# Performance work log

Measured on AMD Instinct MI355X. Metric: run time of the kernel, lower is better.

## Reference

```python
import jax, jax.numpy as jnp
import numpy as np

B, L, DIN, H, E, K = 64, 256, 768, 64, 8, 2
S = 16  # sqrt(L): token<->feature grid side
LOSS_COEF = 1e-2


def gelu(x):
    return jax.nn.gelu(x, approximate=False)  # torch nn.GELU (exact erf)


def cv_squared(v):
    v = v.astype(jnp.float32)
    return jnp.var(v, ddof=1) / (jnp.mean(v) ** 2 + 1e-10)


def setup_inputs() -> dict:
    key = jax.random.key(0)
    ks = jax.random.split(key, 16)
    rn = lambda k, shape, s=0.02: jax.random.normal(k, shape, jnp.float32) * s
    lap = jnp.array([[0., 1., 0.], [1., -4., 1.], [0., 1., 0.]], jnp.float32)
    return {
        "x": jax.random.normal(ks[0], (B, L, DIN), jnp.float32),
        "dte": jax.random.normal(ks[1], (B, L, DIN), jnp.float32),
        "w_gate": rn(ks[2], (L, E), 1.0),
        "W_exp": rn(ks[3], (E, DIN, H)), "b_exp": jnp.zeros((E, H), jnp.float32),
        "W_sh": rn(ks[4], (DIN, H)), "b_sh": jnp.zeros((H,), jnp.float32),
        "ln_g": jnp.ones((H,), jnp.float32), "ln_b": jnp.zeros((H,), jnp.float32),
        "W_px": rn(ks[5], (H, 2 * H)), "b_px": jnp.zeros((2 * H,), jnp.float32),
        "conv_sh": jnp.tile(lap[None, None], (H, 1, 1, 1)),  # depthwise Laplacian [H,1,3,3]
        "W_pxx": rn(ks[6], (H, H)), "b_pxx": jnp.zeros((H,), jnp.float32),
        "W_dte": rn(ks[7], (H, H)), "b_dte": jnp.zeros((H,), jnp.float32),
        "W_dteall": rn(ks[8], (H, H)), "b_dteall": jnp.zeros((H,), jnp.float32),
        "W_rgb": rn(ks[9], (DIN, H)), "b_rgb": jnp.zeros((H,), jnp.float32),
        "W_fx": rn(ks[10], (H, H)), "b_fx": jnp.zeros((H,), jnp.float32),
        "W_fmod": rn(ks[11], (H, H)), "b_fmod": jnp.zeros((H,), jnp.float32),
        "W_fxx": rn(ks[12], (H, H)), "b_fxx": jnp.zeros((H,), jnp.float32),
    }


def reference(x, dte, w_gate, W_exp, b_exp, W_sh, b_sh, ln_g, ln_b, W_px, b_px,
              conv_sh, W_pxx, b_pxx, W_dte, b_dte, W_dteall, b_dteall,
              W_rgb, b_rgb, W_fx, b_fx, W_fmod, b_fmod, W_fxx, b_fxx):
    # ---- top-k gating (clean logits; noisy_gating=False / eval) ----
    logits = dte.mean(-1) @ w_gate                     # [B,E]
    topv, topi = jax.lax.top_k(logits, K)
    topg = jax.nn.softmax(topv, axis=1)
    gates = jnp.zeros_like(logits).at[jnp.arange(B)[:, None], topi].set(topg)
    importance = gates.sum(0)
    load = (gates > 0).sum(0).astype(jnp.float32)
    loss = LOSS_COEF * (cv_squared(importance) + cv_squared(load))
    # ---- sparse dispatch / expert Linear / weighted combine (dense-equivalent) ----
    y = jnp.einsum('be,bld,edh->blh', gates, dte, W_exp) + (gates @ b_exp)[:, None, :]
    # ---- shared expert Linear + Shared block ----
    sh = dte @ W_sh + b_sh                             # [B,L,H]
    shortcut = sh
    t = (sh - sh.mean(-1, keepdims=True)) * jax.lax.rsqrt(sh.var(-1, keepdims=True) + 1e-6)
    t = t * ln_g + ln_b
    t = t @ W_px + b_px                                # [B,L,2H]
    t1, t2 = t[..., :H], t[..., H:]
    f = t1.transpose(0, 2, 1).reshape(B, H, S, S)      # token2feature
    f = jax.lax.conv_general_dilated(f, conv_sh, (1, 1), 'SAME', feature_group_count=H)
    t1 = f.reshape(B, H, L).transpose(0, 2, 1)         # feature2token
    sh = (gelu(t1) * t2) @ W_pxx + b_pxx + shortcut
    # ---- combine MoE and shared streams ----
    dte_tok = (y @ W_dte + b_dte) + (sh @ W_dteall + b_dteall)
    rgb_tok = x @ W_rgb + b_rgb
    # ---- Fusion (its self.norm was overwritten to GELU; token<->feature round-trip is identity) ----
    shortcut = rgb_tok
    a = gelu(rgb_tok) @ W_fx + b_fx
    m = gelu(dte_tok) @ W_fmod + b_fmod
    out = (gelu(m) * a) @ W_fxx + b_fxx + shortcut     # [B,L,H]
    return out, loss
```

## Files before the change

kernel.cpp:

```cpp
#include <hip/hip_runtime.h>
#include <math.h>

typedef unsigned short u16;
typedef unsigned int u32;


__device__ __forceinline__ float bf2f(u16 u) {
    union { u32 i; float f; } x; x.i = ((u32)u) << 16; return x.f;
}
__device__ __forceinline__ u16 f2bf(float f) {
    union { float f; u32 i; } x; x.f = f;
    u32 i = x.i;
    return (u16)((i + 0x7fffu + ((i >> 16) & 1u)) >> 16);
}
__device__ __forceinline__ u32 pack2(float a, float b) {
    return (u32)f2bf(a) | ((u32)f2bf(b) << 16);
}
__device__ __forceinline__ float wsum(float v) {
    #pragma unroll
    for (int o = 1; o < 64; o <<= 1) v += __shfl_xor(v, o, 64);
    return v;
}
__device__ __forceinline__ float gelu_f(float x) {
    return 0.5f * x * (1.0f + erff(x * 0.70710678118654752440f));
}

__global__ __launch_bounds__(256) void k_gate_part(const float* __restrict__ dte,
                                                   const float* __restrict__ w_gate,
                                                   float* __restrict__ partial) {
    __shared__ float dmeanS[64];
    int p = blockIdx.x, tid = threadIdx.x, w = tid >> 6, lane = tid & 63;
    for (int i = 0; i < 16; i++) {
        int l = w * 16 + i;
        const float* pr = dte + ((size_t)p * 64 + l) * 768;
        float s = 0.f;
        #pragma unroll
        for (int j = 0; j < 12; j++) s += pr[j * 64 + lane];
        s = wsum(s);
        if (lane == 0) dmeanS[l] = s * (1.f / 768.f);
    }
    __syncthreads();
    if (w == 0) {
        float dm = dmeanS[lane];
        int wl = (p & 3) * 64 + lane;
        #pragma unroll
        for (int e = 0; e < 8; e++) {
            float s = wsum(dm * w_gate[wl * 8 + e]);
            if (lane == 0) partial[p * 8 + e] = s;
        }
    }
}

__global__ __launch_bounds__(256) void k_gate_fin(const float* __restrict__ partial,
                                                  const float* __restrict__ b_exp,
                                                  int* __restrict__ topi,
                                                  float* __restrict__ topg,
                                                  float* __restrict__ bias_y,
                                                  float* __restrict__ loss_out) {
    __shared__ float gS[64 * 8];
    __shared__ int i0S[64], i1S[64];
    __shared__ float g0S[64], g1S[64];
    int tid = threadIdx.x;
    if (tid < 64) {
        float lg[8];
        #pragma unroll
        for (int e = 0; e < 8; e++)
            lg[e] = partial[(tid * 4 + 0) * 8 + e] + partial[(tid * 4 + 1) * 8 + e] +
                    partial[(tid * 4 + 2) * 8 + e] + partial[(tid * 4 + 3) * 8 + e];
        int i0 = 0; float v0 = lg[0];
        #pragma unroll
        for (int e = 1; e < 8; e++) if (lg[e] > v0) { v0 = lg[e]; i0 = e; }
        int i1 = -1; float v1 = -1e30f;
        #pragma unroll
        for (int e = 0; e < 8; e++) if (e != i0 && lg[e] > v1) { v1 = lg[e]; i1 = e; }
        if (i1 < 0) i1 = (i0 + 1) & 7;
        float e2 = expf(v1 - v0);
        float g0 = 1.f / (1.f + e2);
        float g1 = e2 / (1.f + e2);
        #pragma unroll
        for (int e = 0; e < 8; e++) gS[tid * 8 + e] = 0.f;
        gS[tid * 8 + i0] = g0;
        gS[tid * 8 + i1] = g1;
        i0S[tid] = i0; i1S[tid] = i1; g0S[tid] = g0; g1S[tid] = g1;
        topi[tid * 2] = i0; topi[tid * 2 + 1] = i1;
        topg[tid * 2] = g0; topg[tid * 2 + 1] = g1;
    }
    __syncthreads();
    for (int idx = tid; idx < 4096; idx += 256) {
        int b = idx >> 6, h = idx & 63;
        bias_y[idx] = g0S[b] * b_exp[i0S[b] * 64 + h] + g1S[b] * b_exp[i1S[b] * 64 + h];
    }
    if (tid < 64) {
        float g[8];
        #pragma unroll
        for (int e = 0; e < 8; e++) g[e] = gS[tid * 8 + e];
        float imp[8], ld[8];
        #pragma unroll
        for (int e = 0; e < 8; e++) {
            imp[e] = wsum(g[e]);
            ld[e]  = wsum(g[e] > 0.f ? 1.f : 0.f);
        }
        if (tid == 0) {
            float l = 0.f;
            {
                float s = 0.f;
                #pragma unroll
                for (int e = 0; e < 8; e++) s += imp[e];
                float mn = s / 8.f, v = 0.f;
                #pragma unroll
                for (int e = 0; e < 8; e++) { float d = imp[e] - mn; v += d * d; }
                l += (v / 7.f) / (mn * mn + 1e-10f);
            }
            {
                float s = 0.f;
                #pragma unroll
                for (int e = 0; e < 8; e++) s += ld[e];
                float mn = s / 8.f, v = 0.f;
                #pragma unroll
                for (int e = 0; e < 8; e++) { float d = ld[e] - mn; v += d * d; }
                l += (v / 7.f) / (mn * mn + 1e-10f);
            }
            loss_out[0] = 0.01f * l;
        }
    }
}

__global__ __launch_bounds__(256) void k_gemm3(const float* __restrict__ dte,
                                               const float* __restrict__ x,
                                               const float* __restrict__ W_sh,
                                               const float* __restrict__ b_sh,
                                               const float* __restrict__ W_exp,
                                               const int* __restrict__ topi,
                                               const float* __restrict__ topg,
                                               const float* __restrict__ bias_y,
                                               const float* __restrict__ W_rgb,
                                               const float* __restrict__ b_rgb,
                                               float* __restrict__ buf_sh,
                                               u16* __restrict__ buf_y,
                                               float* __restrict__ out_rgb) {
    __shared__ float As[64 * 68];
    __shared__ float Ws[64 * 68];
    int bid = blockIdx.x;
    int kind = bid >> 8;
    int row0 = (bid & 255) * 64;
    int b = row0 >> 8;
    int tid = threadIdx.x, rg = tid >> 4, cg = tid & 15;
    const float* A = (kind == 2) ? x : dte;
    const float* W0 = (kind == 2) ? W_rgb : W_sh;
    const float* W1 = W0;
    float g0 = 0.f, g1 = 0.f;
    if (kind == 1) {
        W0 = W_exp + (size_t)topi[2 * b] * 49152;
        W1 = W_exp + (size_t)topi[2 * b + 1] * 49152;
        g0 = topg[2 * b]; g1 = topg[2 * b + 1];
    }
    float acc[4][4] = {};
    for (int kc = 0; kc < 12; kc++) {
        __syncthreads();
        #pragma unroll
        for (int j = 0; j < 4; j++) {
            int e4 = tid + j * 256;
            int r = e4 >> 4, kq = e4 & 15;
            *(float4*)(As + r * 68 + kq * 4) =
                *(const float4*)(A + (size_t)(row0 + r) * 768 + kc * 64 + kq * 4);
        }
        #pragma unroll
        for (int j = 0; j < 4; j++) {
            int e4 = tid + j * 256;
            int k = e4 >> 4, hq = e4 & 15;
            size_t off = (size_t)(kc * 64 + k) * 64 + hq * 4;
            float4 wv;
            if (kind == 1) {
                float4 a = *(const float4*)(W0 + off);
                float4 c = *(const float4*)(W1 + off);
                wv.x = g0 * a.x + g1 * c.x; wv.y = g0 * a.y + g1 * c.y;
                wv.z = g0 * a.z + g1 * c.z; wv.w = g0 * a.w + g1 * c.w;
            } else {
                wv = *(const float4*)(W0 + off);
            }
            *(float4*)(Ws + k * 68 + hq * 4) = wv;
        }
        __syncthreads();
        const float* ar = As + rg * 4 * 68;
        #pragma unroll 8
        for (int kk = 0; kk < 64; kk++) {
            float a0 = ar[kk], a1 = ar[68 + kk], a2 = ar[136 + kk], a3 = ar[204 + kk];
            float4 wv = *(const float4*)(Ws + kk * 68 + cg * 4);
            acc[0][0] += a0 * wv.x; acc[0][1] += a0 * wv.y; acc[0][2] += a0 * wv.z; acc[0][3] += a0 * wv.w;
            acc[1][0] += a1 * wv.x; acc[1][1] += a1 * wv.y; acc[1][2] += a1 * wv.z; acc[1][3] += a1 * wv.w;
            acc[2][0] += a2 * wv.x; acc[2][1] += a2 * wv.y; acc[2][2] += a2 * wv.z; acc[2][3] += a2 * wv.w;
            acc[3][0] += a3 * wv.x; acc[3][1] += a3 * wv.y; acc[3][2] += a3 * wv.z; acc[3][3] += a3 * wv.w;
        }
    }
    if (kind == 0) {
        float4 bs = *(const float4*)(b_sh + cg * 4);
        #pragma unroll
        for (int i = 0; i < 4; i++) {
            int r = row0 + rg * 4 + i;
            *(float4*)(buf_sh + (size_t)r * 64 + cg * 4) =
                make_float4(acc[i][0] + bs.x, acc[i][1] + bs.y, acc[i][2] + bs.z, acc[i][3] + bs.w);
        }
    } else if (kind == 1) {
        float4 by = *(const float4*)(bias_y + b * 64 + cg * 4);
        #pragma unroll
        for (int i = 0; i < 4; i++) {
            int r = row0 + rg * 4 + i;
            u32* dst = (u32*)(buf_y + (size_t)r * 64 + cg * 4);
            dst[0] = pack2(acc[i][0] + by.x, acc[i][1] + by.y);
            dst[1] = pack2(acc[i][2] + by.z, acc[i][3] + by.w);
        }
    } else {
        float4 br = *(const float4*)(b_rgb + cg * 4);
        #pragma unroll
        for (int i = 0; i < 4; i++) {
            int r = row0 + rg * 4 + i;
            *(float4*)(out_rgb + (size_t)r * 64 + cg * 4) =
                make_float4(acc[i][0] + br.x, acc[i][1] + br.y, acc[i][2] + br.z, acc[i][3] + br.w);
        }
    }
}

__global__ __launch_bounds__(256) void k_lnpx(const float* __restrict__ buf_sh,
                                              const float* __restrict__ ln_g,
                                              const float* __restrict__ ln_b,
                                              const float* __restrict__ W_px,
                                              const float* __restrict__ b_px,
                                              u16* __restrict__ t1, u16* __restrict__ t2) {
    __shared__ float T[32 * 68];
    __shared__ float Wpx[8192];
    int r0 = blockIdx.x * 32;
    int tid = threadIdx.x, w = tid >> 6, lane = tid & 63;
    #pragma unroll
    for (int j = 0; j < 8; j++) {
        int e4 = tid + j * 256;
        *(float4*)(Wpx + e4 * 4) = *(const float4*)(W_px + e4 * 4);
    }
    float lnG = ln_g[lane], lnB = ln_b[lane];
    for (int i = 0; i < 8; i++) {
        int l = w * 8 + i;
        float v = buf_sh[(size_t)(r0 + l) * 64 + lane];
        float mean = wsum(v) * (1.f / 64.f);
        float d = v - mean;
        float var = wsum(d * d) * (1.f / 64.f);
        T[l * 68 + lane] = d * rsqrtf(var + 1e-6f) * lnG + lnB;
    }
    __syncthreads();
    int rg = tid >> 4, cg = tid & 15;
    float acc1[2][4] = {}, acc2[2][4] = {};
    const float* tr = T + rg * 2 * 68;
    #pragma unroll 4
    for (int kk = 0; kk < 64; kk++) {
        float a0 = tr[kk], a1 = tr[68 + kk];
        float4 w1 = *(const float4*)(Wpx + kk * 128 + cg * 4);
        float4 w2 = *(const float4*)(Wpx + kk * 128 + 64 + cg * 4);
        acc1[0][0] += a0 * w1.x; acc1[0][1] += a0 * w1.y; acc1[0][2] += a0 * w1.z; acc1[0][3] += a0 * w1.w;
        acc1[1][0] += a1 * w1.x; acc1[1][1] += a1 * w1.y; acc1[1][2] += a1 * w1.z; acc1[1][3] += a1 * w1.w;
        acc2[0][0] += a0 * w2.x; acc2[0][1] += a0 * w2.y; acc2[0][2] += a0 * w2.z; acc2[0][3] += a0 * w2.w;
        acc2[1][0] += a1 * w2.x; acc2[1][1] += a1 * w2.y; acc2[1][2] += a1 * w2.z; acc2[1][3] += a1 * w2.w;
    }
    float4 b1 = *(const float4*)(b_px + cg * 4);
    float4 b2 = *(const float4*)(b_px + 64 + cg * 4);
    #pragma unroll
    for (int i = 0; i < 2; i++) {
        int r = r0 + rg * 2 + i;
        u32* d1 = (u32*)(t1 + (size_t)r * 64 + cg * 4);
        d1[0] = pack2(acc1[i][0] + b1.x, acc1[i][1] + b1.y);
        d1[1] = pack2(acc1[i][2] + b1.z, acc1[i][3] + b1.w);
        u32* d2 = (u32*)(t2 + (size_t)r * 64 + cg * 4);
        d2[0] = pack2(acc2[i][0] + b2.x, acc2[i][1] + b2.y);
        d2[1] = pack2(acc2[i][2] + b2.z, acc2[i][3] + b2.w);
    }
}

__global__ __launch_bounds__(256) void k_tail(const u16* __restrict__ t1,
                                              const u16* __restrict__ t2,
                                              const float* __restrict__ conv_sh,
                                              const float* __restrict__ W_pxx,
                                              const float* __restrict__ b_pxx,
                                              const float* __restrict__ buf_sh,
                                              const u16* __restrict__ buf_y,
                                              const float* __restrict__ W_dte,
                                              const float* __restrict__ b_dte,
                                              const float* __restrict__ W_dteall,
                                              const float* __restrict__ b_dteall,
                                              const float* __restrict__ W_fx,
                                              const float* __restrict__ b_fx,
                                              const float* __restrict__ W_fmod,
                                              const float* __restrict__ b_fmod,
                                              const float* __restrict__ W_fxx,
                                              const float* __restrict__ b_fxx,
                                              float* __restrict__ out) {
    __shared__ float B0[32 * 68];
    __shared__ float B1[32 * 68];
    __shared__ float B2[32 * 68];
    __shared__ float RS[32 * 64];
    int r0 = blockIdx.x * 32;
    int tid = threadIdx.x, w = tid >> 6, lane = tid & 63;
    int rg = tid >> 4, cg = tid & 15;

    {
        float c0 = conv_sh[lane * 9 + 0], c1 = conv_sh[lane * 9 + 1], c2 = conv_sh[lane * 9 + 2];
        float c3 = conv_sh[lane * 9 + 3], c4 = conv_sh[lane * 9 + 4], c5 = conv_sh[lane * 9 + 5];
        float c6 = conv_sh[lane * 9 + 6], c7 = conv_sh[lane * 9 + 7], c8 = conv_sh[lane * 9 + 8];
        for (int i = 0; i < 8; i++) {
            int l = w * 8 + i;
            int gr = r0 + l;
            int pix = gr & 255, ii = pix >> 4, jj = pix & 15;
            const u16* p = t1 + (size_t)gr * 64 + lane;
            float c = c4 * bf2f(p[0]);
            if (ii > 0) {
                c += c1 * bf2f(p[-1024]);
                if (jj > 0)  c += c0 * bf2f(p[-1024 - 64]);
                if (jj < 15) c += c2 * bf2f(p[-1024 + 64]);
            }
            if (jj > 0)  c += c3 * bf2f(p[-64]);
            if (jj < 15) c += c5 * bf2f(p[64]);
            if (ii < 15) {
                c += c7 * bf2f(p[1024]);
                if (jj > 0)  c += c6 * bf2f(p[1024 - 64]);
                if (jj < 15) c += c8 * bf2f(p[1024 + 64]);
            }
            B0[l * 68 + lane] = gelu_f(c) * bf2f(t2[(size_t)gr * 64 + lane]);
        }
    }
    __syncthreads();

    {
        float acc[2][4] = {};
        const float* ur = B0 + rg * 2 * 68;
        #pragma unroll 8
        for (int kk = 0; kk < 64; kk++) {
            float a0 = ur[kk], a1 = ur[68 + kk];
            float4 wv = *(const float4*)(W_pxx + kk * 64 + cg * 4);
            acc[0][0] += a0 * wv.x; acc[0][1] += a0 * wv.y; acc[0][2] += a0 * wv.z; acc[0][3] += a0 * wv.w;
            acc[1][0] += a1 * wv.x; acc[1][1] += a1 * wv.y; acc[1][2] += a1 * wv.z; acc[1][3] += a1 * wv.w;
        }
        float4 bp = *(const float4*)(b_pxx + cg * 4);
        #pragma unroll
        for (int i = 0; i < 2; i++) {
            int lr = rg * 2 + i;
            float4 shv = *(const float4*)(buf_sh + (size_t)(r0 + lr) * 64 + cg * 4);
            *(float4*)(B1 + lr * 68 + cg * 4) =
                make_float4(acc[i][0] + bp.x + shv.x, acc[i][1] + bp.y + shv.y,
                            acc[i][2] + bp.z + shv.z, acc[i][3] + bp.w + shv.w);
        }
    }
    __syncthreads();

    #pragma unroll
    for (int j = 0; j < 8; j++) {
        int e = tid + j * 256;
        int l = e >> 6, c = e & 63;
        B0[l * 68 + c] = bf2f(buf_y[(size_t)(r0 + l) * 64 + c]);
    }
    __syncthreads();

    {
        float acc[2][4] = {};
        const float* yr = B0 + rg * 2 * 68;
        const float* sr = B1 + rg * 2 * 68;
        #pragma unroll 4
        for (int kk = 0; kk < 64; kk++) {
            float y0 = yr[kk], y1 = yr[68 + kk];
            float s0 = sr[kk], s1 = sr[68 + kk];
            float4 w1 = *(const float4*)(W_dte + kk * 64 + cg * 4);
            float4 w2 = *(const float4*)(W_dteall + kk * 64 + cg * 4);
            acc[0][0] += y0 * w1.x + s0 * w2.x; acc[0][1] += y0 * w1.y + s0 * w2.y;
            acc[0][2] += y0 * w1.z + s0 * w2.z; acc[0][3] += y0 * w1.w + s0 * w2.w;
            acc[1][0] += y1 * w1.x + s1 * w2.x; acc[1][1] += y1 * w1.y + s1 * w2.y;
            acc[1][2] += y1 * w1.z + s1 * w2.z; acc[1][3] += y1 * w1.w + s1 * w2.w;
        }
        float4 bd1 = *(const float4*)(b_dte + cg * 4);
        float4 bd2 = *(const float4*)(b_dteall + cg * 4);
        #pragma unroll
        for (int i = 0; i < 2; i++) {
            int lr = rg * 2 + i;
            *(float4*)(B2 + lr * 68 + cg * 4) =
                make_float4(gelu_f(acc[i][0] + bd1.x + bd2.x), gelu_f(acc[i][1] + bd1.y + bd2.y),
                            gelu_f(acc[i][2] + bd1.z + bd2.z), gelu_f(acc[i][3] + bd1.w + bd2.w));
        }
    }
    __syncthreads();

    #pragma unroll
    for (int j = 0; j < 2; j++) {
        int e4 = tid + j * 256;
        int l = e4 >> 4, c4i = e4 & 15;
        float4 rv = *(const float4*)(out + (size_t)(r0 + l) * 64 + c4i * 4);
        *(float4*)(RS + l * 64 + c4i * 4) = rv;
        B1[l * 68 + c4i * 4 + 0] = gelu_f(rv.x);
        B1[l * 68 + c4i * 4 + 1] = gelu_f(rv.y);
        B1[l * 68 + c4i * 4 + 2] = gelu_f(rv.z);
        B1[l * 68 + c4i * 4 + 3] = gelu_f(rv.w);
    }
    __syncthreads();

    {
        float accA[2][4] = {}, accM[2][4] = {};
        const float* ga = B1 + rg * 2 * 68;
        const float* gm = B2 + rg * 2 * 68;
        #pragma unroll 4
        for (int kk = 0; kk < 64; kk++) {
            float a0 = ga[kk], a1 = ga[68 + kk];
            float m0 = gm[kk], m1 = gm[68 + kk];
            float4 wa = *(const float4*)(W_fx + kk * 64 + cg * 4);
            float4 wm = *(const float4*)(W_fmod + kk * 64 + cg * 4);
            accA[0][0] += a0 * wa.x; accA[0][1] += a0 * wa.y; accA[0][2] += a0 * wa.z; accA[0][3] += a0 * wa.w;
            accA[1][0] += a1 * wa.x; accA[1][1] += a1 * wa.y; accA[1][2] += a1 * wa.z; accA[1][3] += a1 * wa.w;
            accM[0][0] += m0 * wm.x; accM[0][1] += m0 * wm.y; accM[0][2] += m0 * wm.z; accM[0][3] += m0 * wm.w;
            accM[1][0] += m1 * wm.x; accM[1][1] += m1 * wm.y; accM[1][2] += m1 * wm.z; accM[1][3] += m1 * wm.w;
        }
        float4 bx = *(const float4*)(b_fx + cg * 4);
        float4 bm = *(const float4*)(b_fmod + cg * 4);
        #pragma unroll
        for (int i = 0; i < 2; i++) {
            int lr = rg * 2 + i;
            float a0 = accA[i][0] + bx.x, a1 = accA[i][1] + bx.y, a2 = accA[i][2] + bx.z, a3 = accA[i][3] + bx.w;
            float m0 = accM[i][0] + bm.x, m1 = accM[i][1] + bm.y, m2 = accM[i][2] + bm.z, m3 = accM[i][3] + bm.w;
            *(float4*)(B0 + lr * 68 + cg * 4) =
                make_float4(gelu_f(m0) * a0, gelu_f(m1) * a1, gelu_f(m2) * a2, gelu_f(m3) * a3);
        }
    }
    __syncthreads();

    {
        float acc[2][4] = {};
        const float* pr = B0 + rg * 2 * 68;
        #pragma unroll 8
        for (int kk = 0; kk < 64; kk++) {
            float p0 = pr[kk], p1 = pr[68 + kk];
            float4 wv = *(const float4*)(W_fxx + kk * 64 + cg * 4);
            acc[0][0] += p0 * wv.x; acc[0][1] += p0 * wv.y; acc[0][2] += p0 * wv.z; acc[0][3] += p0 * wv.w;
            acc[1][0] += p1 * wv.x; acc[1][1] += p1 * wv.y; acc[1][2] += p1 * wv.z; acc[1][3] += p1 * wv.w;
        }
        float4 bo = *(const float4*)(b_fxx + cg * 4);
        #pragma unroll
        for (int i = 0; i < 2; i++) {
            int lr = rg * 2 + i;
            *(float4*)(out + (size_t)(r0 + lr) * 64 + cg * 4) =
                make_float4(acc[i][0] + bo.x + RS[lr * 64 + cg * 4 + 0],
                            acc[i][1] + bo.y + RS[lr * 64 + cg * 4 + 1],
                            acc[i][2] + bo.z + RS[lr * 64 + cg * 4 + 2],
                            acc[i][3] + bo.w + RS[lr * 64 + cg * 4 + 3]);
        }
    }
}

extern "C" void kernel_launch(void* const* d_in, const int* in_sizes, int n_in,
                              void* d_out, int out_size, void* d_ws, size_t ws_size,
                              hipStream_t stream) {
    const float* x       = (const float*)d_in[0];
    const float* dte     = (const float*)d_in[1];
    const float* w_gate  = (const float*)d_in[2];
    const float* W_exp   = (const float*)d_in[3];
    const float* b_exp   = (const float*)d_in[4];
    const float* W_sh    = (const float*)d_in[5];
    const float* b_sh    = (const float*)d_in[6];
    const float* ln_g    = (const float*)d_in[7];
    const float* ln_b    = (const float*)d_in[8];
    const float* W_px    = (const float*)d_in[9];
    const float* b_px    = (const float*)d_in[10];
    const float* conv_sh = (const float*)d_in[11];
    const float* W_pxx   = (const float*)d_in[12];
    const float* b_pxx   = (const float*)d_in[13];
    const float* W_dte   = (const float*)d_in[14];
    const float* b_dte   = (const float*)d_in[15];
    const float* W_dteall= (const float*)d_in[16];
    const float* b_dteall= (const float*)d_in[17];
    const float* W_rgb   = (const float*)d_in[18];
    const float* b_rgb   = (const float*)d_in[19];
    const float* W_fx    = (const float*)d_in[20];
    const float* b_fx    = (const float*)d_in[21];
    const float* W_fmod  = (const float*)d_in[22];
    const float* b_fmod  = (const float*)d_in[23];
    const float* W_fxx   = (const float*)d_in[24];
    const float* b_fxx   = (const float*)d_in[25];

    float* out = (float*)d_out;

    float* wsf    = (float*)d_ws;
    float* partial= wsf;
    int*   topi   = (int*)(wsf + 2048);
    float* topg   = wsf + 2176;
    float* bias_y = wsf + 2304;
    float* buf_sh = wsf + 8192;
    u16*   buf_y  = (u16*)(wsf + 8192 + 1048576);
    u16*   t1     = (u16*)(wsf + 8192 + 1048576 + 524288);
    u16*   t2     = (u16*)(wsf + 8192 + 1048576 + 524288*2);

    hipLaunchKernelGGL(k_gate_part, dim3(256), dim3(256), 0, stream, dte, w_gate, partial);
    hipLaunchKernelGGL(k_gate_fin, dim3(1), dim3(256), 0, stream,
                       partial, b_exp, topi, topg, bias_y, out + 1048576);
    hipLaunchKernelGGL(k_gemm3, dim3(768), dim3(256), 0, stream,
                       dte, x, W_sh, b_sh, W_exp, topi, topg, bias_y, W_rgb, b_rgb,
                       buf_sh, buf_y, out);
    hipLaunchKernelGGL(k_lnpx, dim3(512), dim3(256), 0, stream,
                       buf_sh, ln_g, ln_b, W_px, b_px, t1, t2);
    hipLaunchKernelGGL(k_tail, dim3(512), dim3(256), 0, stream,
                       t1, t2, conv_sh, W_pxx, b_pxx, buf_sh, buf_y,
                       W_dte, b_dte, W_dteall, b_dteall,
                       W_fx, b_fx, W_fmod, b_fmod, W_fxx, b_fxx, out);

    (void)in_sizes; (void)n_in; (void)out_size; (void)ws_size;
}
```

Baseline: 292.8 us.

## Use bf16 MFMA for the three big projection GEMMs and vectorize gate reduction

The fused dte/x projection GEMM (shared, mixed-expert, rgb) now converts A and W tiles to bf16 in shared memory and computes with 16x16x32 bf16 MFMA instructions instead of scalar FP32 FMAs, using a K-chunk of 32. Block ordering interleaves the shared and expert kinds. The gate-mean reduction now uses float4 loads. The FP32 GEMM is the dominant compute cost. The trade-off is reduced precision from the bf16 inputs, scalar strided stores into the transposed W tile, and twice as many sync rounds.

Measured after the change: 278.7 us. 4.8% less time.

```diff
diff --git a/kernel.cpp b/kernel.cpp
--- a/kernel.cpp
+++ b/kernel.cpp
@@ -3,6 +3,8 @@
 
 typedef unsigned short u16;
 typedef unsigned int u32;
+typedef __attribute__((ext_vector_type(8))) short bf16x8;
+typedef __attribute__((ext_vector_type(4))) float f32x4;
 
 
 __device__ __forceinline__ float bf2f(u16 u) {
@@ -35,7 +37,10 @@
         const float* pr = dte + ((size_t)p * 64 + l) * 768;
         float s = 0.f;
         #pragma unroll
-        for (int j = 0; j < 12; j++) s += pr[j * 64 + lane];
+        for (int j = 0; j < 3; j++) {
+            float4 v = *(const float4*)(pr + (lane + j * 64) * 4);
+            s += v.x + v.y + v.z + v.w;
+        }
         s = wsum(s);
         if (lane == 0) dmeanS[l] = s * (1.f / 768.f);
     }
@@ -138,13 +143,16 @@
                                                float* __restrict__ buf_sh,
                                                u16* __restrict__ buf_y,
                                                float* __restrict__ out_rgb) {
-    __shared__ float As[64 * 68];
-    __shared__ float Ws[64 * 68];
+    __shared__ u16 As[64 * 40];
+    __shared__ u16 Wt[64 * 40];
     int bid = blockIdx.x;
-    int kind = bid >> 8;
-    int row0 = (bid & 255) * 64;
+    int kind, row0;
+    if (bid < 512) { kind = bid & 1; row0 = (bid >> 1) * 64; }
+    else           { kind = 2;       row0 = (bid - 512) * 64; }
     int b = row0 >> 8;
-    int tid = threadIdx.x, rg = tid >> 4, cg = tid & 15;
+    int tid = threadIdx.x, wv = tid >> 6, lane = tid & 63;
+    int m = lane & 15, quad = lane >> 4;
+
     const float* A = (kind == 2) ? x : dte;
     const float* W0 = (kind == 2) ? W_rgb : W_sh;
     const float* W1 = W0;
@@ -154,68 +162,66 @@
         W1 = W_exp + (size_t)topi[2 * b + 1] * 49152;
         g0 = topg[2 * b]; g1 = topg[2 * b + 1];
     }
-    float acc[4][4] = {};
-    for (int kc = 0; kc < 12; kc++) {
+
+    f32x4 acc0 = {0.f, 0.f, 0.f, 0.f}, acc1 = acc0, acc2 = acc0, acc3 = acc0;
+
+    for (int kc = 0; kc < 24; kc++) {
         __syncthreads();
         #pragma unroll
-        for (int j = 0; j < 4; j++) {
+        for (int j = 0; j < 2; j++) {
             int e4 = tid + j * 256;
-            int r = e4 >> 4, kq = e4 & 15;
-            *(float4*)(As + r * 68 + kq * 4) =
-                *(const float4*)(A + (size_t)(row0 + r) * 768 + kc * 64 + kq * 4);
-        }
-        #pragma unroll
-        for (int j = 0; j < 4; j++) {
+            int r = e4 >> 3, kq = e4 & 7;
+            float4 v = *(const float4*)(A + (size_t)(row0 + r) * 768 + kc * 32 + kq * 4);
+            u32* d = (u32*)&As[r * 40 + kq * 4];
+            d[0] = pack2(v.x, v.y);
+            d[1] = pack2(v.z, v.w);
+        }
+        #pragma unroll
+        for (int j = 0; j < 2; j++) {
             int e4 = tid + j * 256;
-            int k = e4 >> 4, hq = e4 & 15;
-            size_t off = (size_t)(kc * 64 + k) * 64 + hq * 4;
-            float4 wv;
+            int k = e4 >> 4, n4 = (e4 & 15) * 4;
+            size_t off = (size_t)(kc * 32 + k) * 64 + n4;
+            float4 wvv;
             if (kind == 1) {
                 float4 a = *(const float4*)(W0 + off);
                 float4 c = *(const float4*)(W1 + off);
-                wv.x = g0 * a.x + g1 * c.x; wv.y = g0 * a.y + g1 * c.y;
-                wv.z = g0 * a.z + g1 * c.z; wv.w = g0 * a.w + g1 * c.w;
+                wvv.x = g0 * a.x + g1 * c.x; wvv.y = g0 * a.y + g1 * c.y;
+                wvv.z = g0 * a.z + g1 * c.z; wvv.w = g0 * a.w + g1 * c.w;
             } else {
-                wv = *(const float4*)(W0 + off);
+                wvv = *(const float4*)(W0 + off);
             }
-            *(float4*)(Ws + k * 68 + hq * 4) = wv;
+            Wt[(n4 + 0) * 40 + k] = f2bf(wvv.x);
+            Wt[(n4 + 1) * 40 + k] = f2bf(wvv.y);
+            Wt[(n4 + 2) * 40 + k] = f2bf(wvv.z);
+            Wt[(n4 + 3) * 40 + k] = f2bf(wvv.w);
         }
         __syncthreads();
-        const float* ar = As + rg * 4 * 68;
-        #pragma unroll 8
-        for (int kk = 0; kk < 64; kk++) {
-            float a0 = ar[kk], a1 = ar[68 + kk], a2 = ar[136 + kk], a3 = ar[204 + kk];
-            float4 wv = *(const float4*)(Ws + kk * 68 + cg * 4);
-            acc[0][0] += a0 * wv.x; acc[0][1] += a0 * wv.y; acc[0][2] += a0 * wv.z; acc[0][3] += a0 * wv.w;
-            acc[1][0] += a1 * wv.x; acc[1][1] += a1 * wv.y; acc[1][2] += a1 * wv.z; acc[1][3] += a1 * wv.w;
-            acc[2][0] += a2 * wv.x; acc[2][1] += a2 * wv.y; acc[2][2] += a2 * wv.z; acc[2][3] += a2 * wv.w;
-            acc[3][0] += a3 * wv.x; acc[3][1] += a3 * wv.y; acc[3][2] += a3 * wv.z; acc[3][3] += a3 * wv.w;
-        }
-    }
-    if (kind == 0) {
-        float4 bs = *(const float4*)(b_sh + cg * 4);
+        bf16x8 a = *(const bf16x8*)&As[(wv * 16 + m) * 40 + quad * 8];
+        bf16x8 b0 = *(const bf16x8*)&Wt[(0 * 16 + m) * 40 + quad * 8];
+        bf16x8 b1 = *(const bf16x8*)&Wt[(1 * 16 + m) * 40 + quad * 8];
+        bf16x8 b2 = *(const bf16x8*)&Wt[(2 * 16 + m) * 40 + quad * 8];
+        bf16x8 b3 = *(const bf16x8*)&Wt[(3 * 16 + m) * 40 + quad * 8];
+        acc0 = __builtin_amdgcn_mfma_f32_16x16x32_bf16(a, b0, acc0, 0, 0, 0);
+        acc1 = __builtin_amdgcn_mfma_f32_16x16x32_bf16(a, b1, acc1, 0, 0, 0);
+        acc2 = __builtin_amdgcn_mfma_f32_16x16x32_bf16(a, b2, acc2, 0, 0, 0);
+        acc3 = __builtin_amdgcn_mfma_f32_16x16x32_bf16(a, b3, acc3, 0, 0, 0);
+    }
+
+    f32x4 accs[4] = {acc0, acc1, acc2, acc3};
+    #pragma unroll
+    for (int t = 0; t < 4; t++) {
+        int col = t * 16 + m;
+        float bias;
+        if (kind == 0)      bias = b_sh[col];
+        else if (kind == 1) bias = bias_y[b * 64 + col];
+        else                bias = b_rgb[col];
         #pragma unroll
         for (int i = 0; i < 4; i++) {
-            int r = row0 + rg * 4 + i;
-            *(float4*)(buf_sh + (size_t)r * 64 + cg * 4) =
-                make_float4(acc[i][0] + bs.x, acc[i][1] + bs.y, acc[i][2] + bs.z, acc[i][3] + bs.w);
-        }
-    } else if (kind == 1) {
-        float4 by = *(const float4*)(bias_y + b * 64 + cg * 4);
-        #pragma unroll
-        for (int i = 0; i < 4; i++) {
-            int r = row0 + rg * 4 + i;
-            u32* dst = (u32*)(buf_y + (size_t)r * 64 + cg * 4);
-            dst[0] = pack2(acc[i][0] + by.x, acc[i][1] + by.y);
-            dst[1] = pack2(acc[i][2] + by.z, acc[i][3] + by.w);
-        }
-    } else {
-        float4 br = *(const float4*)(b_rgb + cg * 4);
-        #pragma unroll
-        for (int i = 0; i < 4; i++) {
-            int r = row0 + rg * 4 + i;
-            *(float4*)(out_rgb + (size_t)r * 64 + cg * 4) =
-                make_float4(acc[i][0] + br.x, acc[i][1] + br.y, acc[i][2] + br.z, acc[i][3] + br.w);
+            int r = row0 + wv * 16 + quad * 4 + i;
+            float val = accs[t][i] + bias;
+            if (kind == 0)      buf_sh[(size_t)r * 64 + col] = val;
+            else if (kind == 1) buf_y[(size_t)r * 64 + col] = f2bf(val);
+            else                out_rgb[(size_t)r * 64 + col] = val;
         }
     }
 }
@@ -331,9 +337,9 @@
         #pragma unroll 8
         for (int kk = 0; kk < 64; kk++) {
             float a0 = ur[kk], a1 = ur[68 + kk];
-            float4 wv = *(const float4*)(W_pxx + kk * 64 + cg * 4);
-            acc[0][0] += a0 * wv.x; acc[0][1] += a0 * wv.y; acc[0][2] += a0 * wv.z; acc[0][3] += a0 * wv.w;
-            acc[1][0] += a1 * wv.x; acc[1][1] += a1 * wv.y; acc[1][2] += a1 * wv.z; acc[1][3] += a1 * wv.w;
+            float4 wvv = *(const float4*)(W_pxx + kk * 64 + cg * 4);
+            acc[0][0] += a0 * wvv.x; acc[0][1] += a0 * wvv.y; acc[0][2] += a0 * wvv.z; acc[0][3] += a0 * wvv.w;
+            acc[1][0] += a1 * wvv.x; acc[1][1] += a1 * wvv.y; acc[1][2] += a1 * wvv.z; acc[1][3] += a1 * wvv.w;
         }
         float4 bp = *(const float4*)(b_pxx + cg * 4);
         #pragma unroll
@@ -429,9 +435,9 @@
         #pragma unroll 8
         for (int kk = 0; kk < 64; kk++) {
             float p0 = pr[kk], p1 = pr[68 + kk];
-            float4 wv = *(const float4*)(W_fxx + kk * 64 + cg * 4);
-            acc[0][0] += p0 * wv.x; acc[0][1] += p0 * wv.y; acc[0][2] += p0 * wv.z; acc[0][3] += p0 * wv.w;
-            acc[1][0] += p1 * wv.x; acc[1][1] += p1 * wv.y; acc[1][2] += p1 * wv.z; acc[1][3] += p1 * wv.w;
+            float4 wvv = *(const float4*)(W_fxx + kk * 64 + cg * 4);
+            acc[0][0] += p0 * wvv.x; acc[0][1] += p0 * wvv.y; acc[0][2] += p0 * wvv.z; acc[0][3] += p0 * wvv.w;
+            acc[1][0] += p1 * wvv.x; acc[1][1] += p1 * wvv.y; acc[1][2] += p1 * wvv.z; acc[1][3] += p1 * wvv.w;
         }
         float4 bo = *(const float4*)(b_fxx + cg * 4);
         #pragma unroll
```
